# Optimization experiments

Hardware: AMD Instinct MI355X
Metric: run time of the kernel (lower is better)

## Reference

```python
import jax, jax.numpy as jnp
import numpy as np

EPS = 1e-8
THRESHOLD = 0.5  # ternary quantization threshold

IN_FEATURES = 4096
OUT_FEATURES = 4096


def setup_inputs() -> dict:
    key = jax.random.key(0)
    k_x, k_w, k_b = jax.random.split(key, 3)
    x = jax.random.normal(k_x, (2, 2048, IN_FEATURES), dtype=jnp.float32)
    # xavier_uniform init for weight (out, in)
    limit = float(np.sqrt(6.0 / (IN_FEATURES + OUT_FEATURES)))
    weight = jax.random.uniform(k_w, (OUT_FEATURES, IN_FEATURES), dtype=jnp.float32,
                                minval=-limit, maxval=limit)
    bias = jnp.zeros((OUT_FEATURES,), dtype=jnp.float32)
    return {"x": x, "weight": weight, "bias": bias}


def ternary_quantize(w):
    # scale = mean(|w|), clamped; quantize to {-1,0,1} with 0.5 threshold
    scale = jnp.maximum(jnp.mean(jnp.abs(w)), EPS)
    w_norm = w / scale
    q = jnp.sign(w_norm) * (jnp.abs(w_norm) > THRESHOLD).astype(w.dtype)
    return q, scale


def reference(x, weight, bias):
    # eval-mode forward of BitNetLinear (ternary mode, activation scaling on)
    qw, scale = ternary_quantize(weight)
    input_scale = jnp.maximum(jnp.mean(jnp.abs(x)), EPS)
    scaled_x = x / input_scale
    # F.linear: y = x @ W^T + b, with dequantized weight qw*scale
    out = jnp.einsum('bsi,oi->bso', scaled_x, qw * scale) + bias
    return out * input_scale
```

## Files before the change

### kernel.cpp

```cpp
#include <hip/hip_runtime.h>
#include <hip/hip_bf16.h>

#define AS1 __attribute__((address_space(1)))
#define AS3 __attribute__((address_space(3)))

typedef __attribute__((ext_vector_type(8))) short bfrag8;
typedef __attribute__((ext_vector_type(4))) float floatx4;

static constexpr int M = 4096, N = 4096, K = 4096;
static constexpr long long NELEM = 16777216LL;
static constexpr int PB = 1024;

__device__ __forceinline__ unsigned short f2bf(float f) {
    unsigned int u = __float_as_uint(f);
    u += 0x7FFFu + ((u >> 16) & 1u);
    return (unsigned short)(u >> 16);
}

__device__ __forceinline__ unsigned short tq(float v, float scale_f) {
    float wn = v / scale_f;
    if (fabsf(wn) > 0.5f)
        return (unsigned short)(0x3F80u | ((__float_as_uint(v) >> 16) & 0x8000u));
    return 0;
}

__device__ __forceinline__ double block_reduce(double s) {
    #pragma unroll
    for (int off = 32; off > 0; off >>= 1) s += __shfl_down(s, off, 64);
    __shared__ double part[4];
    int lane = threadIdx.x & 63, wv = threadIdx.x >> 6;
    if (lane == 0) part[wv] = s;
    __syncthreads();
    return part[0] + part[1] + part[2] + part[3];
}

__device__ __forceinline__ void block_reduce2_bcast(double& a, double& b) {
    #pragma unroll
    for (int off = 32; off > 0; off >>= 1) {
        a += __shfl_down(a, off, 64);
        b += __shfl_down(b, off, 64);
    }
    __shared__ double pa[4], pb[4];
    int lane = threadIdx.x & 63, wv = threadIdx.x >> 6;
    if (lane == 0) { pa[wv] = a; pb[wv] = b; }
    __syncthreads();
    a = pa[0] + pa[1] + pa[2] + pa[3];
    b = pb[0] + pb[1] + pb[2] + pb[3];
}

__global__ __launch_bounds__(256) void prep_reduce(
        const float* __restrict__ x, unsigned short* __restrict__ xb,
        const float* __restrict__ w,
        double* __restrict__ px, double* __restrict__ pw) {
    const int b = blockIdx.x;
    const bool isW = b >= PB;
    const int rb = isW ? b - PB : b;
    const float4* src = (const float4*)(isW ? w : x);
    const long long base = (long long)rb * 4096 + threadIdx.x;

    float4 v[16];
    #pragma unroll
    for (int i = 0; i < 16; i++) v[i] = src[base + i * 256];

    double s = 0.0;
    #pragma unroll
    for (int i = 0; i < 16; i++) {
        s += (double)fabsf(v[i].x); s += (double)fabsf(v[i].y);
        s += (double)fabsf(v[i].z); s += (double)fabsf(v[i].w);
    }

    if (!isW) {
        ushort4* xb4 = (ushort4*)xb;
        #pragma unroll
        for (int i = 0; i < 16; i++) {
            ushort4 r;
            r.x = f2bf(v[i].x); r.y = f2bf(v[i].y);
            r.z = f2bf(v[i].z); r.w = f2bf(v[i].w);
            xb4[base + i * 256] = r;
        }
    }

    double bs = block_reduce(s);
    if (threadIdx.x == 0) (isW ? pw : px)[rb] = bs;
}

__global__ __launch_bounds__(256) void quantize_w(
        const float* __restrict__ w, unsigned short* __restrict__ qb,
        const double* __restrict__ px, const double* __restrict__ pw,
        float* __restrict__ scales) {
    const int t = threadIdx.x;
    double sx = 0.0, sw = 0.0;
    #pragma unroll
    for (int i = 0; i < 4; i++) { sx += px[t + i * 256]; sw += pw[t + i * 256]; }
    block_reduce2_bcast(sx, sw);
    const float scale_w = (float)fmax(sw / (double)NELEM, 1e-8);
    const float scale_x = (float)fmax(sx / (double)NELEM, 1e-8);
    if (blockIdx.x == 0 && t == 0) { scales[0] = scale_w; scales[1] = scale_x; }

    const float4* w4 = (const float4*)w;
    ushort4* q4 = (ushort4*)qb;
    const long long base = (long long)blockIdx.x * 4096 + t;
    float4 v[16];
    #pragma unroll
    for (int i = 0; i < 16; i++) v[i] = w4[base + i * 256];
    #pragma unroll
    for (int i = 0; i < 16; i++) {
        ushort4 r;
        r.x = tq(v[i].x, scale_w); r.y = tq(v[i].y, scale_w);
        r.z = tq(v[i].z, scale_w); r.w = tq(v[i].w, scale_w);
        q4[base + i * 256] = r;
    }
}

__global__ __launch_bounds__(512, 2) void gemm_bt256(
        const unsigned short* __restrict__ A,
        const unsigned short* __restrict__ B,
        const float* __restrict__ bias,
        const float* __restrict__ scales,
        float* __restrict__ out) {
    __shared__ alignas(16) char lds[131072];

    const int tid = threadIdx.x;
    const int lane = tid & 63;
    const int wv = tid >> 6;
    const int wm = wv & 1;
    const int wn = wv >> 1;
    const int col16 = lane & 15;
    const int quad  = lane >> 4;

    const int bid = blockIdx.x;
    const int swz = (bid & 7) * 32 + (bid >> 3);
    const int bx = swz & 15;
    const int by = swz >> 4;
    const int m0 = by * 256;
    const int n0 = bx * 256;

    const int srow8  = lane >> 3;
    const int schunk = (lane & 7) ^ srow8;
    const int scol   = schunk * 8;

    floatx4 acc[8][4];
    #pragma unroll
    for (int i = 0; i < 8; i++)
        #pragma unroll
        for (int j = 0; j < 4; j++)
            acc[i][j] = (floatx4)0.0f;

    char* buf0 = (char*)lds;
    char* buf1 = (char*)lds + 65536;

    auto stage_half = [&](const unsigned short* __restrict__ gmat, int base0,
                          char* region, long long k0, int h) {
        #pragma unroll
        for (int l = 0; l < 2; ++l) {
            const int c = wv * 2 + l;
            const unsigned short* g = gmat
                + (size_t)(base0 + h * 128 + c * 8 + srow8) * (size_t)K
                + (size_t)k0 + scol;
            char* d = region + h * 16384 + c * 1024 + lane * 16;
            __builtin_amdgcn_global_load_lds((const AS1 void*)g, (AS3 void*)d, 16, 0, 0);
        }
    };

    stage_half(B, n0, buf0 + 32768, 0, 0);
    stage_half(B, n0, buf0 + 32768, 0, 1);
    stage_half(A, m0, buf0,         0, 0);
    stage_half(A, m0, buf0,         0, 1);
    stage_half(B, n0, buf1 + 32768, 64, 0);
    stage_half(B, n0, buf1 + 32768, 64, 1);
    asm volatile("s_waitcnt vmcnt(4)" ::: "memory");
    __builtin_amdgcn_s_barrier();

    auto tile_body = [&](char* bufc, char* bufn, int t) {
        const bool stA = (t + 1) < 64;
        const bool stB = (t + 2) < 64;
        const long long kA = (long long)(t + 1) * 64;
        const long long kB = (long long)(t + 2) * 64;
        const char* bA = bufc;
        const char* bB = bufc + 32768;

        bfrag8 bf[4][2];
        #pragma unroll
        for (int j = 0; j < 4; ++j) {
            const int rB = wn * 64 + j * 16 + col16;
            #pragma unroll
            for (int kk = 0; kk < 2; ++kk)
                bf[j][kk] = *(const bfrag8*)(bB + rB * 128 +
                                (((kk * 4 + quad) ^ (col16 & 7)) << 4));
        }

        #pragma unroll
        for (int q = 0; q < 4; ++q) {
            bfrag8 af[2][2];
            #pragma unroll
            for (int di = 0; di < 2; ++di) {
                const int rA = wm * 128 + (q * 2 + di) * 16 + col16;
                #pragma unroll
                for (int kk = 0; kk < 2; ++kk)
                    af[di][kk] = *(const bfrag8*)(bA + rA * 128 +
                                    (((kk * 4 + quad) ^ (col16 & 7)) << 4));
            }
            if (q == 0 && stA) stage_half(A, m0, bufn, kA, 0);
            if (q == 1 && stA) stage_half(A, m0, bufn, kA, 1);
            if (q == 2 && stB) stage_half(B, n0, bufc + 32768, kB, 0);
            if (q == 3 && stB) stage_half(B, n0, bufc + 32768, kB, 1);

            __builtin_amdgcn_s_barrier();
            asm volatile("s_waitcnt lgkmcnt(0)" ::: "memory");
            __builtin_amdgcn_s_setprio(1);
            #pragma unroll
            for (int di = 0; di < 2; ++di)
                #pragma unroll
                for (int j = 0; j < 4; ++j) {
                    acc[q * 2 + di][j] = __builtin_amdgcn_mfma_f32_16x16x32_bf16(
                        af[di][0], bf[j][0], acc[q * 2 + di][j], 0, 0, 0);
                    acc[q * 2 + di][j] = __builtin_amdgcn_mfma_f32_16x16x32_bf16(
                        af[di][1], bf[j][1], acc[q * 2 + di][j], 0, 0, 0);
                }
            __builtin_amdgcn_s_setprio(0);
            if (q == 3) asm volatile("s_waitcnt vmcnt(4)" ::: "memory");
            __builtin_amdgcn_s_barrier();
        }
    };

    for (int t2 = 0; t2 < 32; ++t2) {
        tile_body(buf0, buf1, 2 * t2);
        tile_body(buf1, buf0, 2 * t2 + 1);
    }

    const float wscale = scales[0];
    const float iscale = scales[1];

    float bv[4];
    #pragma unroll
    for (int j = 0; j < 4; ++j)
        bv[j] = bias[n0 + wn * 64 + j * 16 + col16] * iscale;

    #pragma unroll
    for (int i = 0; i < 8; ++i) {
        const int mbase = m0 + wm * 128 + i * 16 + quad * 4;
        #pragma unroll
        for (int j = 0; j < 4; ++j) {
            const int n = n0 + wn * 64 + j * 16 + col16;
            #pragma unroll
            for (int r = 0; r < 4; ++r)
                out[(size_t)(mbase + r) * N + n] = acc[i][j][r] * wscale + bv[j];
        }
    }
}

extern "C" void kernel_launch(void* const* d_in, const int* in_sizes, int n_in,
                              void* d_out, int out_size, void* d_ws, size_t ws_size,
                              hipStream_t stream) {
    const float* x    = (const float*)d_in[0];
    const float* w    = (const float*)d_in[1];
    const float* bias = (const float*)d_in[2];
    float* out = (float*)d_out;

    char* ws = (char*)d_ws;
    float*  scales = (float*)ws;
    double* px     = (double*)(ws + 256);
    double* pw     = (double*)(ws + 256 + PB * 8);
    unsigned short* xb = (unsigned short*)(ws + 16640);
    unsigned short* qb = (unsigned short*)(ws + 16640 + (size_t)NELEM * 2);

    prep_reduce<<<2 * PB, 256, 0, stream>>>(x, xb, w, px, pw);
    quantize_w<<<PB, 256, 0, stream>>>(w, qb, px, pw, scales);

    gemm_bt256<<<dim3(256), 512, 0, stream>>>(xb, qb, bias, scales, out);
}
```

Before: 287.5 us.

## Merge reduction and weight quantization into one kernel with a grid barrier

Replaces the two prep kernels with a single kernel. Each block reduces both x and w, converts x to bf16, then waits at a software grid-wide barrier built from an atomic counter before it computes the global scales and quantizes its slice of w. This removes one kernel launch and its boundary, and the second read of w may hit in cache. The barrier relies on all 1024 blocks being resident at the same time (launch_bounds 256,4) and adds a memset launch plus atomic spinning, which risks deadlock if occupancy is lower than assumed.

```diff
diff --git a/kernel.cpp b/kernel.cpp
--- a/kernel.cpp
+++ b/kernel.cpp
@@ -22,16 +22,6 @@
     if (fabsf(wn) > 0.5f)
         return (unsigned short)(0x3F80u | ((__float_as_uint(v) >> 16) & 0x8000u));
     return 0;
-}
-
-__device__ __forceinline__ double block_reduce(double s) {
-    #pragma unroll
-    for (int off = 32; off > 0; off >>= 1) s += __shfl_down(s, off, 64);
-    __shared__ double part[4];
-    int lane = threadIdx.x & 63, wv = threadIdx.x >> 6;
-    if (lane == 0) part[wv] = s;
-    __syncthreads();
-    return part[0] + part[1] + part[2] + part[3];
 }
 
 __device__ __forceinline__ void block_reduce2_bcast(double& a, double& b) {
@@ -48,66 +38,67 @@
     b = pb[0] + pb[1] + pb[2] + pb[3];
 }
 
-__global__ __launch_bounds__(256) void prep_reduce(
+__global__ __launch_bounds__(256, 4) void prep_coop(
         const float* __restrict__ x, unsigned short* __restrict__ xb,
-        const float* __restrict__ w,
-        double* __restrict__ px, double* __restrict__ pw) {
+        const float* __restrict__ w, unsigned short* __restrict__ qb,
+        double* __restrict__ px, double* __restrict__ pw,
+        float* __restrict__ scales, unsigned int* __restrict__ bc) {
+    const int t = threadIdx.x;
     const int b = blockIdx.x;
-    const bool isW = b >= PB;
-    const int rb = isW ? b - PB : b;
-    const float4* src = (const float4*)(isW ? w : x);
-    const long long base = (long long)rb * 4096 + threadIdx.x;
-
-    float4 v[16];
-    #pragma unroll
-    for (int i = 0; i < 16; i++) v[i] = src[base + i * 256];
-
-    double s = 0.0;
+    const long long base = (long long)b * 4096 + t;
+
+    const float4* x4 = (const float4*)x;
+    ushort4* xb4 = (ushort4*)xb;
+    double sx = 0.0;
     #pragma unroll
     for (int i = 0; i < 16; i++) {
-        s += (double)fabsf(v[i].x); s += (double)fabsf(v[i].y);
-        s += (double)fabsf(v[i].z); s += (double)fabsf(v[i].w);
-    }
-
-    if (!isW) {
-        ushort4* xb4 = (ushort4*)xb;
-        #pragma unroll
-        for (int i = 0; i < 16; i++) {
-            ushort4 r;
-            r.x = f2bf(v[i].x); r.y = f2bf(v[i].y);
-            r.z = f2bf(v[i].z); r.w = f2bf(v[i].w);
-            xb4[base + i * 256] = r;
-        }
-    }
-
-    double bs = block_reduce(s);
-    if (threadIdx.x == 0) (isW ? pw : px)[rb] = bs;
-}
-
-__global__ __launch_bounds__(256) void quantize_w(
-        const float* __restrict__ w, unsigned short* __restrict__ qb,
-        const double* __restrict__ px, const double* __restrict__ pw,
-        float* __restrict__ scales) {
-    const int t = threadIdx.x;
-    double sx = 0.0, sw = 0.0;
-    #pragma unroll
-    for (int i = 0; i < 4; i++) { sx += px[t + i * 256]; sw += pw[t + i * 256]; }
+        float4 v = x4[base + i * 256];
+        sx += (double)fabsf(v.x); sx += (double)fabsf(v.y);
+        sx += (double)fabsf(v.z); sx += (double)fabsf(v.w);
+        ushort4 r;
+        r.x = f2bf(v.x); r.y = f2bf(v.y);
+        r.z = f2bf(v.z); r.w = f2bf(v.w);
+        xb4[base + i * 256] = r;
+    }
+
+    const float4* w4 = (const float4*)w;
+    double sw = 0.0;
+    #pragma unroll
+    for (int i = 0; i < 16; i++) {
+        float4 v = w4[base + i * 256];
+        sw += (double)fabsf(v.x); sw += (double)fabsf(v.y);
+        sw += (double)fabsf(v.z); sw += (double)fabsf(v.w);
+    }
+
     block_reduce2_bcast(sx, sw);
-    const float scale_w = (float)fmax(sw / (double)NELEM, 1e-8);
-    const float scale_x = (float)fmax(sx / (double)NELEM, 1e-8);
-    if (blockIdx.x == 0 && t == 0) { scales[0] = scale_w; scales[1] = scale_x; }
-
-    const float4* w4 = (const float4*)w;
+    if (t == 0) { px[b] = sx; pw[b] = sw; }
+
+    if (t == 0) {
+        __threadfence();
+        atomicAdd(bc, 1u);
+        while (atomicAdd(bc, 0u) < (unsigned)gridDim.x)
+            __builtin_amdgcn_s_sleep(2);
+        __threadfence();
+    }
+    __syncthreads();
+
+    double fx = 0.0, fw = 0.0;
+    #pragma unroll
+    for (int i = 0; i < 4; i++) { fx += px[t + i * 256]; fw += pw[t + i * 256]; }
+    block_reduce2_bcast(fx, fw);
+    const float scale_w = (float)fmax(fw / (double)NELEM, 1e-8);
+    const float scale_x = (float)fmax(fx / (double)NELEM, 1e-8);
+    if (b == 0 && t == 0) { scales[0] = scale_w; scales[1] = scale_x; }
+
     ushort4* q4 = (ushort4*)qb;
-    const long long base = (long long)blockIdx.x * 4096 + t;
-    float4 v[16];
-    #pragma unroll
-    for (int i = 0; i < 16; i++) v[i] = w4[base + i * 256];
+    float4 vv[16];
+    #pragma unroll
+    for (int i = 0; i < 16; i++) vv[i] = w4[base + i * 256];
     #pragma unroll
     for (int i = 0; i < 16; i++) {
         ushort4 r;
-        r.x = tq(v[i].x, scale_w); r.y = tq(v[i].y, scale_w);
-        r.z = tq(v[i].z, scale_w); r.w = tq(v[i].w, scale_w);
+        r.x = tq(vv[i].x, scale_w); r.y = tq(vv[i].y, scale_w);
+        r.z = tq(vv[i].z, scale_w); r.w = tq(vv[i].w, scale_w);
         q4[base + i * 256] = r;
     }
 }
@@ -259,13 +250,13 @@
 
     char* ws = (char*)d_ws;
     float*  scales = (float*)ws;
+    unsigned int* bc = (unsigned int*)(ws + 64);
     double* px     = (double*)(ws + 256);
     double* pw     = (double*)(ws + 256 + PB * 8);
     unsigned short* xb = (unsigned short*)(ws + 16640);
     unsigned short* qb = (unsigned short*)(ws + 16640 + (size_t)NELEM * 2);
 
-    prep_reduce<<<2 * PB, 256, 0, stream>>>(x, xb, w, px, pw);
-    quantize_w<<<PB, 256, 0, stream>>>(w, qb, px, pw, scales);
-
+    hipMemsetAsync(bc, 0, sizeof(unsigned int), stream);
+    prep_coop<<<PB, 256, 0, stream>>>(x, xb, w, qb, px, pw, scales, bc);
     gemm_bt256<<<dim3(256), 512, 0, stream>>>(xb, qb, bias, scales, out);
 }
```

Result: slower. 428.9 us (+49.2%).

## Restructure GEMM tile pipeline to prefetch two K-tiles ahead for both operands

Applied to the files above, without the earlier changes.

The staging schedule changes so that both A and B tiles for step t+2 are loaded into the buffer just consumed. Before, A was staged one step ahead into the other buffer and B two steps ahead. A-fragment LDS reads are now spread across four phases, with global loads interleaved between the MFMA groups. The vmcnt waits are adjusted to keep more loads in flight. The aim is to hide global memory latency better, at the cost of more outstanding loads and changed barrier placement, which risks LDS races if a buffer is overwritten while other waves still read it.

```diff
diff --git a/kernel.cpp b/kernel.cpp
--- a/kernel.cpp
+++ b/kernel.cpp
@@ -162,24 +162,42 @@
         }
     };
 
+    #define LGKM0   asm volatile("s_waitcnt lgkmcnt(0)" ::: "memory")
+    #define BARRIER __builtin_amdgcn_s_barrier()
+
+    #define MFMA_PAIR(rbase, fa0, fa1)                                                 \
+        __builtin_amdgcn_s_setprio(1);                                                 \
+        _Pragma("unroll")                                                              \
+        for (int j = 0; j < 4; ++j) {                                                  \
+            acc[(rbase)][j] = __builtin_amdgcn_mfma_f32_16x16x32_bf16(                 \
+                (fa0)[0], bf[j][0], acc[(rbase)][j], 0, 0, 0);                         \
+            acc[(rbase)][j] = __builtin_amdgcn_mfma_f32_16x16x32_bf16(                 \
+                (fa0)[1], bf[j][1], acc[(rbase)][j], 0, 0, 0);                         \
+            acc[(rbase)+1][j] = __builtin_amdgcn_mfma_f32_16x16x32_bf16(               \
+                (fa1)[0], bf[j][0], acc[(rbase)+1][j], 0, 0, 0);                       \
+            acc[(rbase)+1][j] = __builtin_amdgcn_mfma_f32_16x16x32_bf16(               \
+                (fa1)[1], bf[j][1], acc[(rbase)+1][j], 0, 0, 0);                       \
+        }                                                                              \
+        __builtin_amdgcn_s_setprio(0)
+
     stage_half(B, n0, buf0 + 32768, 0, 0);
     stage_half(B, n0, buf0 + 32768, 0, 1);
     stage_half(A, m0, buf0,         0, 0);
     stage_half(A, m0, buf0,         0, 1);
     stage_half(B, n0, buf1 + 32768, 64, 0);
     stage_half(B, n0, buf1 + 32768, 64, 1);
-    asm volatile("s_waitcnt vmcnt(4)" ::: "memory");
-    __builtin_amdgcn_s_barrier();
-
-    auto tile_body = [&](char* bufc, char* bufn, int t) {
-        const bool stA = (t + 1) < 64;
-        const bool stB = (t + 2) < 64;
-        const long long kA = (long long)(t + 1) * 64;
-        const long long kB = (long long)(t + 2) * 64;
+    stage_half(A, m0, buf1,         64, 0);
+    stage_half(A, m0, buf1,         64, 1);
+    asm volatile("s_waitcnt vmcnt(8)" ::: "memory");
+    BARRIER;
+
+    auto tile_body = [&](char* bufc, int t) {
+        const bool st = (t + 2) < 64;
+        const long long kN = (long long)(t + 2) * 64;
         const char* bA = bufc;
         const char* bB = bufc + 32768;
-
-        bfrag8 bf[4][2];
+        bfrag8 bf[4][2], af[4][2];
+
         #pragma unroll
         for (int j = 0; j < 4; ++j) {
             const int rB = wn * 64 + j * 16 + col16;
@@ -188,44 +206,58 @@
                 bf[j][kk] = *(const bfrag8*)(bB + rB * 128 +
                                 (((kk * 4 + quad) ^ (col16 & 7)) << 4));
         }
-
-        #pragma unroll
-        for (int q = 0; q < 4; ++q) {
-            bfrag8 af[2][2];
-            #pragma unroll
-            for (int di = 0; di < 2; ++di) {
-                const int rA = wm * 128 + (q * 2 + di) * 16 + col16;
-                #pragma unroll
-                for (int kk = 0; kk < 2; ++kk)
-                    af[di][kk] = *(const bfrag8*)(bA + rA * 128 +
-                                    (((kk * 4 + quad) ^ (col16 & 7)) << 4));
-            }
-            if (q == 0 && stA) stage_half(A, m0, bufn, kA, 0);
-            if (q == 1 && stA) stage_half(A, m0, bufn, kA, 1);
-            if (q == 2 && stB) stage_half(B, n0, bufc + 32768, kB, 0);
-            if (q == 3 && stB) stage_half(B, n0, bufc + 32768, kB, 1);
-
-            __builtin_amdgcn_s_barrier();
-            asm volatile("s_waitcnt lgkmcnt(0)" ::: "memory");
-            __builtin_amdgcn_s_setprio(1);
-            #pragma unroll
-            for (int di = 0; di < 2; ++di)
-                #pragma unroll
-                for (int j = 0; j < 4; ++j) {
-                    acc[q * 2 + di][j] = __builtin_amdgcn_mfma_f32_16x16x32_bf16(
-                        af[di][0], bf[j][0], acc[q * 2 + di][j], 0, 0, 0);
-                    acc[q * 2 + di][j] = __builtin_amdgcn_mfma_f32_16x16x32_bf16(
-                        af[di][1], bf[j][1], acc[q * 2 + di][j], 0, 0, 0);
-                }
-            __builtin_amdgcn_s_setprio(0);
-            if (q == 3) asm volatile("s_waitcnt vmcnt(4)" ::: "memory");
-            __builtin_amdgcn_s_barrier();
-        }
+        #pragma unroll
+        for (int r = 0; r < 2; ++r) {
+            const int rA = wm * 128 + r * 16 + col16;
+            #pragma unroll
+            for (int kk = 0; kk < 2; ++kk)
+                af[r][kk] = *(const bfrag8*)(bA + rA * 128 +
+                                (((kk * 4 + quad) ^ (col16 & 7)) << 4));
+        }
+        BARRIER; LGKM0;
+        MFMA_PAIR(0, af[0], af[1]);
+        BARRIER;
+
+        #pragma unroll
+        for (int r = 2; r < 4; ++r) {
+            const int rA = wm * 128 + r * 16 + col16;
+            #pragma unroll
+            for (int kk = 0; kk < 2; ++kk)
+                af[r][kk] = *(const bfrag8*)(bA + rA * 128 +
+                                (((kk * 4 + quad) ^ (col16 & 7)) << 4));
+        }
+        if (st) stage_half(B, n0, bufc + 32768, kN, 0);
+        BARRIER; LGKM0;
+        MFMA_PAIR(2, af[2], af[3]);
+        BARRIER;
+
+        #pragma unroll
+        for (int r = 0; r < 4; ++r) {
+            const int rA = wm * 128 + (4 + r) * 16 + col16;
+            #pragma unroll
+            for (int kk = 0; kk < 2; ++kk)
+                af[r][kk] = *(const bfrag8*)(bA + rA * 128 +
+                                (((kk * 4 + quad) ^ (col16 & 7)) << 4));
+        }
+        if (st) stage_half(B, n0, bufc + 32768, kN, 1);
+        BARRIER; LGKM0;
+        MFMA_PAIR(4, af[0], af[1]);
+        BARRIER;
+
+        if (st) {
+            stage_half(A, m0, bufc, kN, 0);
+            stage_half(A, m0, bufc, kN, 1);
+        }
+        BARRIER; LGKM0;
+        MFMA_PAIR(6, af[2], af[3]);
+        if (t < 62)       asm volatile("s_waitcnt vmcnt(8)" ::: "memory");
+        else if (t == 62) asm volatile("s_waitcnt vmcnt(0)" ::: "memory");
+        BARRIER;
     };
 
     for (int t2 = 0; t2 < 32; ++t2) {
-        tile_body(buf0, buf1, 2 * t2);
-        tile_body(buf1, buf0, 2 * t2 + 1);
+        tile_body(buf0, 2 * t2);
+        tile_body(buf1, 2 * t2 + 1);
     }
 
     const float wscale = scales[0];
@@ -247,6 +279,9 @@
                 out[(size_t)(mbase + r) * N + n] = acc[i][j][r] * wscale + bv[j];
         }
     }
+    #undef MFMA_PAIR
+    #undef LGKM0
+    #undef BARRIER
 }
 
 extern "C" void kernel_launch(void* const* d_in, const int* in_sizes, int n_in,
```

After: 317.9 us. 10.6% more time.
